# Kernel tuning notes

Hardware: AMD Instinct MI355X
Metric: run time of the kernel (lower is better)

Reference implementation:

```python
import jax, jax.numpy as jnp
import numpy as np

B, A, C, L, NH, SCALE = 1, 5, 64, 4, 8, 2
H = W = 24
S = 2 * C
KS = 5


def layernorm(x, g, b, eps=1e-5):
    m = x.mean(-1, keepdims=True)
    v = ((x - m) ** 2).mean(-1, keepdims=True)
    return (x - m) * jax.lax.rsqrt(v + eps) * g + b


def pe_1d(n, d):
    # PositionEncoding: temperature**(2*(i//2)/d), sin of even cols then cos of odd cols
    g = jnp.arange(d, dtype=jnp.float32)
    g = 10000.0 ** (2.0 * jnp.floor(g / 2.0) / d)
    p = jnp.arange(n, dtype=jnp.float32)[:, None] / g[None, :]
    return jnp.concatenate([jnp.sin(p[:, 0::2]), jnp.cos(p[:, 1::2])], axis=1)  # [n, d]


def mha(qk, v, in_w, out_w, nh, mask=None):
    # qk, v: [Lq, Bt, D]; torch nn.MultiheadAttention, bias-free, q=k=qk, value=v
    Lq, Bt, D = qk.shape
    dh = D // nh
    wq, wk, wv = jnp.split(in_w, 3, axis=0)
    q = (qk @ wq.T).reshape(Lq, Bt, nh, dh)
    k = (qk @ wk.T).reshape(Lq, Bt, nh, dh)
    vv = (v @ wv.T).reshape(Lq, Bt, nh, dh)
    s = jnp.einsum('lbhd,mbhd->bhlm', q, k) / jnp.sqrt(jnp.float32(dh))
    if mask is not None:
        s = s + mask
    a = jax.nn.softmax(s, axis=-1)
    o = jnp.einsum('bhlm,mbhd->lbhd', a, vv).reshape(Lq, Bt, D)
    return o @ out_w.T


def unfold3x3(x):
    # F.unfold(k=3, pad=1).permute(2,0,1): [N,c,h,w] -> [h*w, N, 9c] (c, kh, kw ordering)
    N, c, h, w = x.shape
    xp = jnp.pad(x, ((0, 0), (0, 0), (1, 1), (1, 1)))
    p = jnp.stack([xp[:, :, i:i + h, j:j + w] for i in range(3) for j in range(3)], axis=2)
    return p.reshape(N, c * 9, h * w).transpose(2, 0, 1)


def conv_hw(x5, w):
    # Conv3d kernel (1,3,3) pad (0,1,1): 2D conv per angular view
    Bc, Ci, Aa, h, w_ = x5.shape
    y = jax.lax.conv_general_dilated(
        x5.transpose(0, 2, 1, 3, 4).reshape(Bc * Aa, Ci, h, w_), w, (1, 1), ((1, 1), (1, 1)),
        dimension_numbers=('NCHW', 'OIHW', 'NCHW'))
    return y.reshape(Bc, Aa, w.shape[0], h, w_).transpose(0, 2, 1, 3, 4)


def window_mask(h, w, k):
    # SpaTrans.gen_mask: additive -inf outside a k x k local window
    kl, kr = k // 2, k - k // 2
    i = jnp.arange(h)
    j = jnp.arange(w)
    mh = (i[None, :] >= i[:, None] - kl) & (i[None, :] < i[:, None] + kr)
    mw = (j[None, :] >= j[:, None] - kl) & (j[None, :] < j[:, None] + kr)
    m = (mh[:, None, :, None] & mw[None, :, None, :]).reshape(h * w, h * w)
    return jnp.where(m, 0.0, -jnp.inf).astype(jnp.float32)


def setup_inputs() -> dict:
    key = jax.random.key(0)
    ks = iter(jax.random.split(key, 64))
    def nrm(shape, s=0.02):
        return jax.random.normal(next(ks), shape, dtype=jnp.float32) * s
    d = {}
    d['lr'] = jax.random.normal(next(ks), (B, 1, A * H, A * W), dtype=jnp.float32)
    Hh, Wh = H * SCALE, W * SCALE
    ch = -1.0 + (2.0 * jnp.arange(Hh, dtype=jnp.float32) + 1.0) / Hh
    cw = -1.0 + (2.0 * jnp.arange(Wh, dtype=jnp.float32) + 1.0) / Wh
    g = jnp.stack(jnp.meshgrid(ch, cw, indexing='ij'), axis=-1).reshape(-1, 2)
    d['coord'] = jnp.broadcast_to(g, (B, Hh * Wh, 2))
    d['conv0_w'] = nrm((C, 1, 3, 3), 0.1)
    d['convi_w'] = nrm((3, C, C, 3, 3), 0.05)
    d['ang_ln_g'] = jnp.ones((L, C)); d['ang_ln_b'] = jnp.zeros((L, C))
    d['ang_in'] = nrm((L, 3 * C, C)); d['ang_out'] = nrm((L, C, C))
    d['ang_ff_g'] = jnp.ones((L, C)); d['ang_ff_b'] = jnp.zeros((L, C))
    d['ang_w1'] = nrm((L, 2 * C, C)); d['ang_w2'] = nrm((L, C, 2 * C))
    d['spa_mlp'] = nrm((L, S, 9 * C))
    d['spa_ln_g'] = jnp.ones((L, S)); d['spa_ln_b'] = jnp.zeros((L, S))
    d['spa_in'] = nrm((L, 3 * S, S)); d['spa_out'] = nrm((L, S, S))
    d['spa_ff_g'] = jnp.ones((L, S)); d['spa_ff_b'] = jnp.zeros((L, S))
    d['spa_w1'] = nrm((L, 2 * S, S)); d['spa_w2'] = nrm((L, S, 2 * S))
    d['spa_lin'] = nrm((L, C, S))
    IN = A * A * C + 2 + 2 * A * A
    d['imp_w0'] = nrm((320, IN)); d['imp_b0'] = jnp.zeros((320,))
    d['imp_w1'] = nrm((320, 320)); d['imp_b1'] = jnp.zeros((320,))
    d['imp_w2'] = nrm((3 * A * A, 320)); d['imp_b2'] = jnp.zeros((3 * A * A,))
    return d


def reference(lr, coord, conv0_w, convi_w, ang_ln_g, ang_ln_b, ang_in, ang_out,
              ang_ff_g, ang_ff_b, ang_w1, ang_w2, spa_mlp, spa_ln_g, spa_ln_b,
              spa_in, spa_out, spa_ff_g, spa_ff_b, spa_w1, spa_w2, spa_lin,
              imp_w0, imp_b0, imp_w1, imp_b1, imp_w2, imp_b2):
    Bn = lr.shape[0]
    # 'b c (a1 h) (a2 w) -> b c (a1 a2) h w'
    x = lr.reshape(Bn, 1, A, H, A, W).transpose(0, 1, 2, 4, 3, 5).reshape(Bn, 1, A * A, H, W)
    spa_pe_img = ((pe_1d(H, C)[:, None, :] + pe_1d(W, C)[None, :, :]) * 0.5).transpose(2, 0, 1)[None]  # [1,C,h,w]
    ang_pe = pe_1d(A * A, C)[:, None, :]  # [A^2,1,C]
    buf = conv_hw(x, conv0_w)
    t = buf
    for i in range(3):
        t = jax.nn.leaky_relu(conv_hw(t, convi_w[i]), 0.2)
    buf = t + buf
    mask = window_mask(H, W, KS)
    blk = buf
    for l in range(L):
        # ---- AngTrans: tokens [A^2, B*h*w, C]
        tok = blk.transpose(2, 0, 3, 4, 1).reshape(A * A, Bn * H * W, C)
        tn = layernorm(tok + ang_pe, ang_ln_g[l], ang_ln_b[l])
        tok = mha(tn, tok, ang_in[l], ang_out[l], NH) + tok
        ff = layernorm(tok, ang_ff_g[l], ang_ff_b[l])
        tok = jax.nn.relu(ff @ ang_w1[l].T) @ ang_w2[l].T + tok
        blk = tok.reshape(A * A, Bn, H, W, C).transpose(1, 4, 0, 2, 3)
        # ---- SpaTrans: tokens [h*w, B*A^2, 2C] with local-window mask
        xb = blk.transpose(0, 2, 1, 3, 4).reshape(Bn * A * A, C, H, W)
        tok = unfold3x3(xb) @ spa_mlp[l].T
        pe_tok = unfold3x3(spa_pe_img) @ spa_mlp[l].T
        tn = layernorm(tok + pe_tok, spa_ln_g[l], spa_ln_b[l])
        tok = mha(tn, tok, spa_in[l], spa_out[l], NH, mask) + tok
        ff = layernorm(tok, spa_ff_g[l], spa_ff_b[l])
        tok = jax.nn.relu(ff @ spa_w1[l].T) @ spa_w2[l].T + tok
        t5 = tok.reshape(H, W, Bn, A * A, S).transpose(2, 4, 3, 0, 1)  # b s a h w
        blk = jnp.einsum('os,bsahw->boahw', spa_lin[l], t5)  # 1x1x1 Conv3d
    buf = blk + buf
    # 'b c (a1 a2) h w -> b c (a1 h) (a2 w)'
    feat_lr = buf.reshape(Bn, C, A, A, H, W).transpose(0, 1, 2, 4, 3, 5).reshape(Bn, C, A * H, A * W)
    Hh, Wh = H * SCALE, W * SCALE
    # per-view bilinear upsample (align_corners=False)
    v = feat_lr.reshape(Bn, C, A, H, A, W).transpose(0, 2, 4, 1, 3, 5).reshape(Bn * A * A, C, H, W)
    v = jax.image.resize(v, (Bn * A * A, C, Hh, Wh), method='bilinear')
    feat_hr = v.reshape(Bn, A, A, C, Hh, Wh).transpose(0, 4, 5, 1, 2, 3).reshape(Bn, Hh, Wh, A * A * C)
    # nearest grid_sample of LR cell-center coords -> relative coord
    c_ = jnp.clip(coord + 1e-6, -1 + 1e-6, 1 - 1e-6)
    ih = jnp.clip(jnp.round(((c_[..., 0] + 1) * H - 1) / 2), 0, H - 1)
    iw = jnp.clip(jnp.round(((c_[..., 1] + 1) * W - 1) / 2), 0, W - 1)
    qh = -1.0 + (2.0 * ih + 1.0) / H
    qw = -1.0 + (2.0 * iw + 1.0) / W
    rel = jnp.stack([(coord[..., 0] - qh) * H, (coord[..., 1] - qw) * W], axis=-1).reshape(Bn, Hh, Wh, 2)
    au = 0.5 + jnp.arange(A, dtype=jnp.float32)  # make_coord ranges [0,A]
    ca = jnp.stack(jnp.meshgrid(au, au, indexing='ij'), axis=-1).reshape(-1)
    ca = jnp.broadcast_to(ca, (Bn, Hh, Wh, 2 * A * A))
    inp = jnp.concatenate([feat_hr, rel, ca], axis=-1)
    h0 = jax.nn.relu(inp @ imp_w0.T + imp_b0)
    h1 = jax.nn.relu(h0 @ imp_w1.T + imp_b1)
    o = h1 @ imp_w2.T + imp_b2
    # 'b h w (a1 a2 c) -> b c (a1 h) (a2 w)', c=3
    return o.reshape(Bn, Hh, Wh, A, A, 3).transpose(0, 5, 3, 1, 4, 2).reshape(Bn, 3, A * Hh, A * Wh)
```

## Files before the change

kernel.cpp:

```cpp
#include <hip/hip_runtime.h>
#include <math.h>

typedef short  s16x4 __attribute__((ext_vector_type(4)));
typedef short  s16x8 __attribute__((ext_vector_type(8)));
typedef float  f32x4 __attribute__((ext_vector_type(4)));

static const size_t PE25_  = 0;
static const size_t SPAPE_ = 2048;
static const size_t X_     = 38912;
static const size_t CAV_   = 53312;
static const size_t PETOK_ = 54272;
static const size_t W9C_   = 349184;
static const size_t W9S_   = 459776;
static const size_t BUF_   = 754688;
static const size_t BLK_   = 1676288;
static const size_t ATOK_  = 2597888;
static const size_t TNF_   = 3519488;
static const size_t STOK_  = 4441088;
static const size_t STOK2_ = 6284288;
static const size_t QKV_   = 9970688;
static const size_t WS_FLOATS = 15500288;
static const size_t T0_ = QKV_ + 2764800;
static const size_t T1_ = T0_ + 921600;
static const size_t ZP_ = QKV_;
static const size_t H0_ = STOK_;
static const size_t H1_ = STOK2_;

__device__ inline ushort f2bf(float x) {
  unsigned u = __float_as_uint(x);
  u += 0x7fffu + ((u >> 16) & 1u);
  return (ushort)(u >> 16);
}
__device__ inline float bf2f(ushort h) { return __uint_as_float(((unsigned)h) << 16); }

__device__ inline void store_split(char* p, f32x4 v) {
  s16x4 hi, lo;
  #pragma unroll
  for (int e = 0; e < 4; ++e) {
    float x = v[e];
    ushort h = f2bf(x);
    ushort l = f2bf(x - bf2f(h));
    hi[e] = (short)h; lo[e] = (short)l;
  }
  *(s16x4*)p = hi;
  *(s16x4*)(p + 1024) = lo;
}

__device__ inline void scatter_split(char* base, int rr, int c6, float v) {
  ushort hi = f2bf(v);
  ushort lo = f2bf(v - bf2f(hi));
  int ks = c6 >> 5, kh = (c6 >> 4) & 1, k4 = (c6 >> 2) & 3;
  int lane2 = (k4 >> 1)*32 + ((rr & 15) << 1) + (k4 & 1);
  int byt = (((rr >> 4)*2 + ks) << 11) + (kh << 9) + (lane2 << 3) + (c6 & 3)*2;
  *(ushort*)(base + byt) = hi;
  *(ushort*)(base + byt + 1024) = lo;
}

__device__ inline void ld_bf16x16(const ushort* p, float* dst) {
  s16x8 a = *(const s16x8*)p;
  s16x8 b = *(const s16x8*)(p + 8);
  #pragma unroll
  for (int e = 0; e < 8; ++e) { dst[e] = bf2f((ushort)a[e]); dst[8 + e] = bf2f((ushort)b[e]); }
}

__device__ inline void slot_decode(int i, int wave, int lane,
                                   int& row, int& kof, int& wo) {
  int idx = (i << 2) + wave;
  int msub = idx >> 2, ks = (idx >> 1) & 1, kh = idx & 1;
  int rsub = (lane >> 1) & 15;
  int ksub = ((lane >> 5) << 3) + ((lane & 1) << 2);
  row = (msub << 4) + rsub;
  kof = (ks << 5) + (kh << 4) + ksub;
  wo = ((msub * 2 + ks) << 11) + (kh << 9) + (lane << 3);
}

__device__ inline void mfma_step(const char* ldsA, const char* ldsB, int lane,
                                 int wr, int wc, f32x4 acc[2][2]) {
  #pragma unroll
  for (int ks = 0; ks < 2; ++ks) {
    s16x8 ah[2], al[2], bh[2], bl[2];
    #pragma unroll
    for (int i = 0; i < 2; ++i) {
      const char* pa = ldsA + (((wr*2 + i)*2 + ks) << 11) + (lane << 4);
      ah[i] = *(const s16x8*)pa;
      al[i] = *(const s16x8*)(pa + 1024);
      const char* pb = ldsB + (((wc*2 + i)*2 + ks) << 11) + (lane << 4);
      bh[i] = *(const s16x8*)pb;
      bl[i] = *(const s16x8*)(pb + 1024);
    }
    #pragma unroll
    for (int i = 0; i < 2; ++i) {
      #pragma unroll
      for (int j = 0; j < 2; ++j) {
        acc[i][j] = __builtin_amdgcn_mfma_f32_16x16x32_bf16(ah[i], bh[j], acc[i][j], 0, 0, 0);
        acc[i][j] = __builtin_amdgcn_mfma_f32_16x16x32_bf16(ah[i], bl[j], acc[i][j], 0, 0, 0);
        acc[i][j] = __builtin_amdgcn_mfma_f32_16x16x32_bf16(al[i], bh[j], acc[i][j], 0, 0, 0);
      }
    }
  }
}

__device__ inline void epilogue(f32x4 acc[2][2], const float* bias, const float* res,
                                float* out, int N, int m0, int n0,
                                int wr, int wc, int lane, int act) {
  int colb = n0 + wc*32 + (lane & 15);
  int rowb = m0 + wr*32 + ((lane >> 4) << 2);
  #pragma unroll
  for (int j = 0; j < 2; ++j) {
    int cc = colb + j*16;
    if (cc >= N) continue;
    float bv = bias ? bias[cc] : 0.f;
    #pragma unroll
    for (int i = 0; i < 2; ++i) {
      #pragma unroll
      for (int r = 0; r < 4; ++r) {
        int rr = rowb + i*16 + r;
        float v = acc[i][j][r] + bv;
        if (act == 1) v = fmaxf(v, 0.f);
        else if (act == 2) v = v > 0.f ? v : 0.2f*v;
        if (res) v += res[(long)rr*N + cc];
        if (act == 3) {
          int hh = rr / 48, ww2 = rr % 48, q = cc / 3, ch = cc % 3;
          out[ch*57600 + ((q/5)*48 + hh)*240 + (q%5)*48 + ww2] = v;
        } else if (act == 4) {
          ((ushort*)out)[(long)rr*N + cc] = f2bf(v);
        } else {
          out[(long)rr*N + cc] = v;
        }
      }
    }
  }
}

template<int K>
__global__ __launch_bounds__(256) void qkvg_k(
    const float* __restrict__ A, const float* __restrict__ pe, int pe_mode,
    const float* __restrict__ g, const float* __restrict__ bb,
    const float* __restrict__ W, float* __restrict__ out,
    int NTr0, int NTr1, int N, int Mreal, int Mpad) {
  constexpr int NCH = K / 64;
  __shared__ char Apl[NCH * 16384];
  __shared__ char Bp[16384];
  __shared__ float sw_[4][64][2];
  __shared__ float sf_[64][2];
  int bid = blockIdx.x;
  int type = bid / Mpad, m = bid % Mpad;
  if (m >= Mreal) return;
  int m0 = m*64;
  int NTr = type ? NTr1 : NTr0;
  int ntbase = type ? NTr0 : 0;
  int t = threadIdx.x, lane = t & 63, wave = t >> 6;
  int wr = wave >> 1, wc = wave & 1;

  if (type == 0) {
    f32x4 rv[NCH][4];
    float sA[4], sQ[4];
    #pragma unroll
    for (int i = 0; i < 4; ++i) { sA[i] = 0.f; sQ[i] = 0.f; }
    #pragma unroll
    for (int ch = 0; ch < NCH; ++ch)
      #pragma unroll
      for (int i = 0; i < 4; ++i) {
        int row, kof, wo;
        slot_decode(i, wave, lane, row, kof, wo);
        int gk = ch*64 + kof;
        f32x4 av = *(const f32x4*)&A[(long)(m0 + row)*K + gk];
        if (pe_mode == 0)      av += *(const f32x4*)&pe[(long)(m0/576)*K + gk];
        else                   av += *(const f32x4*)&pe[(long)(m0%576 + row)*K + gk];
        rv[ch][i] = av;
        #pragma unroll
        for (int e = 0; e < 4; ++e) { sA[i] += av[e]; sQ[i] = fmaf(av[e], av[e], sQ[i]); }
      }
    #pragma unroll
    for (int i = 0; i < 4; ++i) {
      float s = sA[i], q = sQ[i];
      s += __shfl_xor(s, 1, 64);  q += __shfl_xor(q, 1, 64);
      s += __shfl_xor(s, 32, 64); q += __shfl_xor(q, 32, 64);
      if ((lane & 1) == 0 && lane < 32) {
        int row = i*16 + (lane >> 1);
        sw_[wave][row][0] = s; sw_[wave][row][1] = q;
      }
    }
    __syncthreads();
    if (t < 64) {
      float s = sw_[0][t][0] + sw_[1][t][0] + sw_[2][t][0] + sw_[3][t][0];
      float q = sw_[0][t][1] + sw_[1][t][1] + sw_[2][t][1] + sw_[3][t][1];
      float mean = s / K, var = q / K - mean*mean;
      sf_[t][0] = mean; sf_[t][1] = rsqrtf(var + 1e-5f);
    }
    __syncthreads();
    #pragma unroll
    for (int ch = 0; ch < NCH; ++ch)
      #pragma unroll
      for (int i = 0; i < 4; ++i) {
        int row, kof, wo;
        slot_decode(i, wave, lane, row, kof, wo);
        int gk = ch*64 + kof;
        float mean = sf_[row][0], rstd = sf_[row][1];
        f32x4 gv = *(const f32x4*)&g[gk];
        f32x4 bv = *(const f32x4*)&bb[gk];
        f32x4 nv;
        #pragma unroll
        for (int e = 0; e < 4; ++e) nv[e] = (rv[ch][i][e] - mean)*rstd*gv[e] + bv[e];
        store_split(Apl + ch*16384 + wo, nv);
      }
  } else {
    #pragma unroll
    for (int ch = 0; ch < NCH; ++ch)
      #pragma unroll
      for (int i = 0; i < 4; ++i) {
        int row, kof, wo;
        slot_decode(i, wave, lane, row, kof, wo);
        f32x4 av = *(const f32x4*)&A[(long)(m0 + row)*K + ch*64 + kof];
        store_split(Apl + ch*16384 + wo, av);
      }
  }

  int S = NTr * NCH;
  f32x4 pb[4];
  #pragma unroll
  for (int i = 0; i < 4; ++i) {
    int row, kof, wo;
    slot_decode(i, wave, lane, row, kof, wo);
    pb[i] = *(const f32x4*)&W[(long)(ntbase*64 + row)*K + kof];
  }
  f32x4 acc[2][2];
  #pragma unroll
  for (int i = 0; i < 2; ++i)
    #pragma unroll
    for (int j = 0; j < 2; ++j) acc[i][j] = (f32x4){0.f,0.f,0.f,0.f};
  for (int s = 0; s < S; ++s) {
    int nt = s / NCH, ch = s % NCH;
    __syncthreads();
    #pragma unroll
    for (int i = 0; i < 4; ++i) {
      int row, kof, wo;
      slot_decode(i, wave, lane, row, kof, wo);
      store_split(Bp + wo, pb[i]);
    }
    __syncthreads();
    if (s + 1 < S) {
      int ntn = (s+1) / NCH, chn = (s+1) % NCH;
      #pragma unroll
      for (int i = 0; i < 4; ++i) {
        int row, kof, wo;
        slot_decode(i, wave, lane, row, kof, wo);
        pb[i] = *(const f32x4*)&W[(long)((ntbase+ntn)*64 + row)*K + chn*64 + kof];
      }
    }
    mfma_step(Apl + ch*16384, Bp, lane, wr, wc, acc);
    if (ch == NCH - 1) {
      epilogue(acc, nullptr, nullptr, out, N, m0, (ntbase+nt)*64, wr, wc, lane, 4);
      #pragma unroll
      for (int i = 0; i < 2; ++i)
        #pragma unroll
        for (int j = 0; j < 2; ++j) acc[i][j] = (f32x4){0.f,0.f,0.f,0.f};
    }
  }
}

template<int K, int LN>
__global__ __launch_bounds__(256) void mgemm3_k(
    const float* __restrict__ A, const float* __restrict__ A2, int nsplit,
    const float* __restrict__ pe, int pe_mode,
    const float* __restrict__ g, const float* __restrict__ bb,
    const float* __restrict__ W, const float* __restrict__ bias,
    const float* __restrict__ res, float* __restrict__ out,
    int N, int act, int Mreal, int Mpad) {
  constexpr int NCH = K / 64;
  __shared__ char Apl[NCH * 16384];
  __shared__ char Bp[16384];
  int bid = blockIdx.x;
  int m = bid % Mpad, nt = bid / Mpad;
  if (m >= Mreal) return;
  int m0 = m*64, n0 = nt*64;
  int t = threadIdx.x, lane = t & 63, wave = t >> 6;
  int wr = wave >> 1, wc = wave & 1;
  const float* As = LN ? A2 : A;
  #pragma unroll
  for (int ch = 0; ch < NCH; ++ch)
    #pragma unroll
    for (int i = 0; i < 4; ++i) {
      int row, kof, wo;
      slot_decode(i, wave, lane, row, kof, wo);
      f32x4 av = *(const f32x4*)&As[(long)(m0 + row)*K + ch*64 + kof];
      store_split(Apl + ch*16384 + wo, av);
    }
  f32x4 pb[4];
  #pragma unroll
  for (int i = 0; i < 4; ++i) {
    int row, kof, wo;
    slot_decode(i, wave, lane, row, kof, wo);
    int br = n0 + row;
    pb[i] = (br < N) ? *(const f32x4*)&W[(long)br*K + kof] : (f32x4){0.f,0.f,0.f,0.f};
  }
  __syncthreads();
  f32x4 acc[2][2];
  #pragma unroll
  for (int i = 0; i < 2; ++i)
    #pragma unroll
    for (int j = 0; j < 2; ++j) acc[i][j] = (f32x4){0.f,0.f,0.f,0.f};
  for (int ch = 0; ch < NCH; ++ch) {
    #pragma unroll
    for (int i = 0; i < 4; ++i) {
      int row, kof, wo;
      slot_decode(i, wave, lane, row, kof, wo);
      store_split(Bp + wo, pb[i]);
    }
    __syncthreads();
    if (ch + 1 < NCH) {
      #pragma unroll
      for (int i = 0; i < 4; ++i) {
        int row, kof, wo;
        slot_decode(i, wave, lane, row, kof, wo);
        int br = n0 + row;
        pb[i] = (br < N) ? *(const f32x4*)&W[(long)br*K + (ch+1)*64 + kof]
                         : (f32x4){0.f,0.f,0.f,0.f};
      }
    }
    mfma_step(Apl + ch*16384, Bp, lane, wr, wc, acc);
    if (ch + 1 < NCH) __syncthreads();
  }
  epilogue(acc, bias, res, out, N, m0, n0, wr, wc, lane, act);
}

__global__ __launch_bounds__(256) void cgemm3_k(
    const float* __restrict__ in, const float* __restrict__ W9, long wstride,
    const float* __restrict__ res, float* __restrict__ out, long ostride,
    int N, int act, int Mreal, int Mpad) {
  __shared__ float halo[144 * 68];
  __shared__ char Ap[16384], Bp[16384];
  int bid = blockIdx.x;
  int m = bid % Mpad, nt = bid / Mpad;
  if (m >= Mreal) return;
  int ly = blockIdx.y;
  W9  += (long)ly * wstride;
  out += (long)ly * ostride;
  int m0 = m*64, n0 = nt*64;
  int a = m0 / 576, off = m0 % 576;
  int h_lo = off/24 - 1, h_hi = (off + 63)/24 + 1;
  int RH = h_hi - h_lo + 1;
  int t = threadIdx.x, lane = t & 63, wave = t >> 6;
  int wr = wave >> 1, wc = wave & 1;
  for (int sidx = t; sidx < RH*24*16; sidx += 256) {
    int tokr = sidx >> 4, c4 = (sidx & 15) << 2;
    int h = h_lo + tokr/24, w = tokr % 24;
    f32x4 v = {0.f,0.f,0.f,0.f};
    if ((unsigned)h < 24u) v = *(const f32x4*)&in[(long)(a*576 + h*24 + w)*64 + c4];
    *(f32x4*)&halo[tokr*68 + c4] = v;
  }
  f32x4 pb[4];
  #pragma unroll
  for (int i = 0; i < 4; ++i) {
    int row, kof, wo;
    slot_decode(i, wave, lane, row, kof, wo);
    int br = n0 + row;
    pb[i] = (br < N) ? *(const f32x4*)&W9[(long)br*64 + kof] : (f32x4){0.f,0.f,0.f,0.f};
  }
  __syncthreads();
  f32x4 acc[2][2];
  #pragma unroll
  for (int i = 0; i < 2; ++i)
    #pragma unroll
    for (int j = 0; j < 2; ++j) acc[i][j] = (f32x4){0.f,0.f,0.f,0.f};
  for (int ij = 0; ij < 9; ++ij) {
    int di = ij/3 - 1, dj = ij%3 - 1;
    #pragma unroll
    for (int i = 0; i < 4; ++i) {
      int row, kof, wo;
      slot_decode(i, wave, lane, row, kof, wo);
      int tok = off + row;
      int h2 = tok/24 + di, w2 = tok%24 + dj;
      f32x4 v = {0.f,0.f,0.f,0.f};
      if ((unsigned)h2 < 24u && (unsigned)w2 < 24u)
        v = *(const f32x4*)&halo[((h2 - h_lo)*24 + w2)*68 + kof];
      store_split(Ap + wo, v);
      store_split(Bp + wo, pb[i]);
    }
    __syncthreads();
    if (ij < 8) {
      #pragma unroll
      for (int i = 0; i < 4; ++i) {
        int row, kof, wo;
        slot_decode(i, wave, lane, row, kof, wo);
        int br = n0 + row;
        pb[i] = (br < N) ? *(const f32x4*)&W9[((long)(ij+1)*N + br)*64 + kof]
                         : (f32x4){0.f,0.f,0.f,0.f};
      }
    }
    mfma_step(Ap, Bp, lane, wr, wc, acc);
    if (ij < 8) __syncthreads();
  }
  epilogue(acc, nullptr, res, out, N, m0, n0, wr, wc, lane, act);
}

__global__ __launch_bounds__(256) void ang_mega_k(
    const ushort* __restrict__ qkv, const float* __restrict__ Wout,
    const float* __restrict__ blkr, const float* __restrict__ g,
    const float* __restrict__ bb, float* __restrict__ atok, float* __restrict__ tnf) {
  int hw = blockIdx.x;
  __shared__ float lq[25*192];
  __shared__ float lao[25*64];
  __shared__ float po[25*68];
  __shared__ float wout[64*65];
  __shared__ float st[25][2];
  int t = threadIdx.x;
  for (int idx = t; idx < 600; idx += 256) {
    int a3 = idx / 24, c8 = (idx % 24) * 8;
    s16x8 r = *(const s16x8*)&qkv[(long)(a3*576 + hw)*192 + c8];
    #pragma unroll
    for (int e = 0; e < 8; ++e) lq[a3*192 + c8 + e] = bf2f((ushort)r[e]);
  }
  for (int idx = t; idx < 4096; idx += 256) {
    int c = idx >> 6, d = idx & 63;
    wout[c*65 + d] = Wout[idx];
  }
  __syncthreads();
  if (t < 200) {
    int l = t / 8, head = t & 7;
    const float* q = lq + l*192 + head*8;
    float s[25]; float mx = -1e30f;
    #pragma unroll
    for (int mm = 0; mm < 25; ++mm) {
      const float* kk = lq + mm*192 + 64 + head*8;
      float acc = 0.f;
      #pragma unroll
      for (int d = 0; d < 8; ++d) acc = fmaf(q[d], kk[d], acc);
      acc *= 0.3535533905932738f;
      s[mm] = acc; mx = fmaxf(mx, acc);
    }
    float sum = 0.f;
    #pragma unroll
    for (int mm = 0; mm < 25; ++mm) { s[mm] = expf(s[mm] - mx); sum += s[mm]; }
    float inv = 1.f / sum;
    #pragma unroll
    for (int d = 0; d < 8; ++d) {
      float acc = 0.f;
      #pragma unroll
      for (int mm = 0; mm < 25; ++mm) acc = fmaf(s[mm], lq[mm*192 + 128 + head*8 + d], acc);
      lao[l*64 + head*8 + d] = acc * inv;
    }
  }
  __syncthreads();
  for (int idx = t; idx < 1600; idx += 256) {
    int tok = idx >> 6, c = idx & 63;
    const float* ar = &lao[tok*64];
    const float* wr = &wout[c*65];
    float accp = 0.f;
    #pragma unroll 16
    for (int d = 0; d < 64; ++d) accp = fmaf(ar[d], wr[d], accp);
    po[tok*68 + c] = accp + blkr[(long)(tok*576 + hw)*64 + c];
  }
  __syncthreads();
  if (t < 25) {
    float s = 0.f, q = 0.f;
    for (int c = 0; c < 64; ++c) { float x = po[t*68 + c]; s += x; q = fmaf(x, x, q); }
    float mean = s / 64.f, var = q / 64.f - mean*mean;
    st[t][0] = mean; st[t][1] = rsqrtf(var + 1e-5f);
  }
  __syncthreads();
  for (int idx = t; idx < 1600; idx += 256) {
    int tok = idx >> 6, c = idx & 63;
    float x = po[tok*68 + c];
    long gidx = (long)(tok*576 + hw)*64 + c;
    atok[gidx] = x;
    tnf[gidx] = (x - st[tok][0]) * st[tok][1] * g[c] + bb[c];
  }
}

__global__ __launch_bounds__(256) void ffn_ang_k(
    const float* __restrict__ tnf, const float* __restrict__ w1,
    const float* __restrict__ w2, float* __restrict__ atok,
    int Mreal, int Mpad) {
  __shared__ char Ap[16384], Bp[16384], Hp[2][16384];
  int bid = blockIdx.x;
  int m = bid % Mpad;
  if (m >= Mreal) return;
  int m0 = m*64;
  int t = threadIdx.x, lane = t & 63, wave = t >> 6;
  int wr = wave >> 1, wc = wave & 1;
  #pragma unroll
  for (int i = 0; i < 4; ++i) {
    int row, kof, wo;
    slot_decode(i, wave, lane, row, kof, wo);
    f32x4 av = *(const f32x4*)&tnf[(long)(m0 + row)*64 + kof];
    store_split(Ap + wo, av);
  }
  f32x4 pb[4];
  #pragma unroll
  for (int i = 0; i < 4; ++i) {
    int row, kof, wo;
    slot_decode(i, wave, lane, row, kof, wo);
    pb[i] = *(const f32x4*)&w1[(long)row*64 + kof];
  }
  __syncthreads();
  for (int nt = 0; nt < 2; ++nt) {
    #pragma unroll
    for (int i = 0; i < 4; ++i) {
      int row, kof, wo;
      slot_decode(i, wave, lane, row, kof, wo);
      store_split(Bp + wo, pb[i]);
    }
    __syncthreads();
    #pragma unroll
    for (int i = 0; i < 4; ++i) {
      int row, kof, wo;
      slot_decode(i, wave, lane, row, kof, wo);
      pb[i] = (nt == 0) ? *(const f32x4*)&w1[(long)(64 + row)*64 + kof]
                        : *(const f32x4*)&w2[(long)row*128 + kof];
    }
    f32x4 acc[2][2];
    #pragma unroll
    for (int i = 0; i < 2; ++i)
      #pragma unroll
      for (int j = 0; j < 2; ++j) acc[i][j] = (f32x4){0.f,0.f,0.f,0.f};
    mfma_step(Ap, Bp, lane, wr, wc, acc);
    #pragma unroll
    for (int jj = 0; jj < 2; ++jj)
      #pragma unroll
      for (int ii = 0; ii < 2; ++ii)
        #pragma unroll
        for (int r = 0; r < 4; ++r) {
          int rr = wr*32 + ii*16 + ((lane >> 4) << 2) + r;
          int cc = wc*32 + jj*16 + (lane & 15);
          scatter_split(Hp[nt], rr, cc, fmaxf(acc[ii][jj][r], 0.f));
        }
    __syncthreads();
  }
  f32x4 acc2[2][2];
  #pragma unroll
  for (int i = 0; i < 2; ++i)
    #pragma unroll
    for (int j = 0; j < 2; ++j) acc2[i][j] = (f32x4){0.f,0.f,0.f,0.f};
  for (int ch = 0; ch < 2; ++ch) {
    #pragma unroll
    for (int i = 0; i < 4; ++i) {
      int row, kof, wo;
      slot_decode(i, wave, lane, row, kof, wo);
      store_split(Bp + wo, pb[i]);
    }
    __syncthreads();
    if (ch == 0) {
      #pragma unroll
      for (int i = 0; i < 4; ++i) {
        int row, kof, wo;
        slot_decode(i, wave, lane, row, kof, wo);
        pb[i] = *(const f32x4*)&w2[(long)row*128 + 64 + kof];
      }
    }
    mfma_step(Hp[ch], Bp, lane, wr, wc, acc2);
    if (ch == 0) __syncthreads();
  }
  epilogue(acc2, nullptr, atok, atok, 64, m0, 0, wr, wc, lane, 0);
}

__global__ __launch_bounds__(512) void megaspa_k(
    const ushort* __restrict__ qkv, const float* __restrict__ stok,
    const float* __restrict__ wout, const float* __restrict__ g,
    const float* __restrict__ bb, const float* __restrict__ w1,
    const float* __restrict__ w2, const float* __restrict__ wlin,
    float* __restrict__ outb, int Mreal, int Mpad) {
  __shared__ char Aop[32768];
  __shared__ char SCR[65536];
  __shared__ float Rf[64*132];
  __shared__ float st[64][2];
  int bid = blockIdx.x;
  int m = bid % Mpad;
  if (m >= Mreal) return;
  int m0 = m*64;
  int t = threadIdx.x, lane = t & 63, wave = t >> 6;
  int wgrp = wave >> 2, w4 = wave & 3;
  int wr = w4 >> 1, wc = w4 & 1;
  char* Bp  = SCR + wgrp*16384;
  char* Hp0 = SCR + 32768;
  char* Hp1 = SCR + 49152;
  ushort* KV = (ushort*)SCR;

  for (int idx = t; idx < 2048; idx += 512) {
    int row = idx >> 5, c4 = (idx & 31) << 2;
    *(f32x4*)&Rf[row*132 + c4] = *(const f32x4*)&stok[(long)(m0 + row)*128 + c4];
  }

  int va = m0 / 576, off = m0 % 576;
  int hb = off/24 - 2;
  int he = (off + 63)/24 + 2;
  int RH = he - hb + 1;
  int rr1 = t >> 3, head = t & 7;
  int x = m0 + rr1;
  int hw = x % 576, h = hw / 24, w = hw % 24;
  float qr[16];
  ld_bf16x16(qkv + (long)x*384 + head*16, qr);
  for (int idx = t; idx < RH*24*16; idx += 512) {
    int tokr = idx >> 4, c8 = (idx & 15) << 3;
    int hh2 = hb + tokr/24, ww2 = tokr % 24;
    s16x8 vv = (s16x8){0,0,0,0,0,0,0,0};
    if ((unsigned)hh2 < 24u)
      vv = *(const s16x8*)&qkv[(long)(va*576 + hh2*24 + ww2)*384 + 128 + c8];
    *(s16x8*)&KV[tokr*136 + c8] = vv;
  }
  __syncthreads();
  float s[25]; float mx = -1e30f;
  #pragma unroll
  for (int ro = 0; ro < 5; ++ro) {
    int h2 = h + ro - 2;
    int hrow = h2 - hb;
    #pragma unroll
    for (int co = 0; co < 5; ++co) {
      int w2 = w + co - 2;
      int w2c = min(max(w2, 0), 23);
      const ushort* kp = &KV[(hrow*24 + w2c)*136 + head*16];
      s16x8 k0 = *(const s16x8*)kp;
      s16x8 k1 = *(const s16x8*)(kp + 8);
      float sc = -1e30f;
      if (h2 >= 0 && h2 < 24 && w2 >= 0 && w2 < 24) {
        sc = 0.f;
        #pragma unroll
        for (int d = 0; d < 8; ++d) sc = fmaf(qr[d], bf2f((ushort)k0[d]), sc);
        #pragma unroll
        for (int d = 0; d < 8; ++d) sc = fmaf(qr[8+d], bf2f((ushort)k1[d]), sc);
        sc *= 0.25f;
      }
      s[ro*5 + co] = sc; mx = fmaxf(mx, sc);
    }
  }
  float sum = 0.f;
  #pragma unroll
  for (int i = 0; i < 25; ++i) {
    float e = (s[i] > -1e29f) ? expf(s[i] - mx) : 0.f;
    s[i] = e; sum += e;
  }
  float inv = 1.f / sum;
  __syncthreads();
  for (int idx = t; idx < RH*24*16; idx += 512) {
    int tokr = idx >> 4, c8 = (idx & 15) << 3;
    int hh2 = hb + tokr/24, ww2 = tokr % 24;
    s16x8 vv = (s16x8){0,0,0,0,0,0,0,0};
    if ((unsigned)hh2 < 24u)
      vv = *(const s16x8*)&qkv[(long)(va*576 + hh2*24 + ww2)*384 + 256 + c8];
    *(s16x8*)&KV[tokr*136 + c8] = vv;
  }
  __syncthreads();
  {
    float acc[16];
    #pragma unroll
    for (int d = 0; d < 16; ++d) acc[d] = 0.f;
    #pragma unroll
    for (int ro = 0; ro < 5; ++ro) {
      int h2 = h + ro - 2;
      int hrow = h2 - hb;
      (void)h2;
      #pragma unroll
      for (int co = 0; co < 5; ++co) {
        int w2 = w + co - 2;
        int w2c = min(max(w2, 0), 23);
        const ushort* vp = &KV[(hrow*24 + w2c)*136 + head*16];
        s16x8 v0 = *(const s16x8*)vp;
        s16x8 v1 = *(const s16x8*)(vp + 8);
        float sv = s[ro*5 + co];
        #pragma unroll
        for (int d = 0; d < 8; ++d) acc[d] = fmaf(sv, bf2f((ushort)v0[d]), acc[d]);
        #pragma unroll
        for (int d = 0; d < 8; ++d) acc[8+d] = fmaf(sv, bf2f((ushort)v1[d]), acc[8+d]);
      }
    }
    #pragma unroll
    for (int d = 0; d < 16; ++d) {
      int cc = head*16 + d;
      scatter_split(Aop + (cc >> 6)*16384, rr1, cc & 63, acc[d] * inv);
    }
  }

  {
    int nt = wgrp;
    f32x4 acc[2][2];
    #pragma unroll
    for (int i = 0; i < 2; ++i)
      #pragma unroll
      for (int j = 0; j < 2; ++j) acc[i][j] = (f32x4){0.f,0.f,0.f,0.f};
    for (int ch = 0; ch < 2; ++ch) {
      __syncthreads();
      #pragma unroll
      for (int i = 0; i < 4; ++i) {
        int row, kof, wo;
        slot_decode(i, w4, lane, row, kof, wo);
        f32x4 bv = *(const f32x4*)&wout[(long)(nt*64 + row)*128 + ch*64 + kof];
        store_split(Bp + wo, bv);
      }
      __syncthreads();
      mfma_step(Aop + ch*16384, Bp, lane, wr, wc, acc);
    }
    int colb = nt*64 + wc*32 + (lane & 15);
    int rowb = wr*32 + ((lane >> 4) << 2);
    #pragma unroll
    for (int j = 0; j < 2; ++j)
      #pragma unroll
      for (int i = 0; i < 2; ++i)
        #pragma unroll
        for (int r = 0; r < 4; ++r) {
          int rr = rowb + i*16 + r, cc = colb + j*16;
          Rf[rr*132 + cc] += acc[i][j][r];
        }
  }
  __syncthreads();

  {
    int row = t >> 3, q8 = t & 7;
    const float* yr = &Rf[row*132 + q8*16];
    float sm = 0.f, sq = 0.f;
    #pragma unroll
    for (int j2 = 0; j2 < 16; ++j2) { float xv = yr[j2]; sm += xv; sq = fmaf(xv, xv, sq); }
    sm += __shfl_xor(sm, 1, 64); sq += __shfl_xor(sq, 1, 64);
    sm += __shfl_xor(sm, 2, 64); sq += __shfl_xor(sq, 2, 64);
    sm += __shfl_xor(sm, 4, 64); sq += __shfl_xor(sq, 4, 64);
    if (q8 == 0) {
      float mean = sm / 128.f, var = sq / 128.f - mean*mean;
      st[row][0] = mean; st[row][1] = rsqrtf(var + 1e-5f);
    }
  }
  __syncthreads();
  {
    int ch = wgrp;
    #pragma unroll
    for (int i = 0; i < 4; ++i) {
      int row, kof, wo;
      slot_decode(i, w4, lane, row, kof, wo);
      int gk = ch*64 + kof;
      f32x4 xv = *(const f32x4*)&Rf[row*132 + gk];
      float mean = st[row][0], rstd = st[row][1];
      f32x4 gv = *(const f32x4*)&g[gk];
      f32x4 bv = *(const f32x4*)&bb[gk];
      f32x4 nv;
      #pragma unroll
      for (int e = 0; e < 4; ++e) nv[e] = (xv[e] - mean)*rstd*gv[e] + bv[e];
      store_split(Aop + ch*16384 + wo, nv);
    }
  }

  f32x4 acc2[2][2];
  #pragma unroll
  for (int i = 0; i < 2; ++i)
    #pragma unroll
    for (int j = 0; j < 2; ++j) acc2[i][j] = (f32x4){0.f,0.f,0.f,0.f};
  for (int r = 0; r < 2; ++r) {
    int nt = 2*r + wgrp;
    f32x4 accH[2][2];
    #pragma unroll
    for (int i = 0; i < 2; ++i)
      #pragma unroll
      for (int j = 0; j < 2; ++j) accH[i][j] = (f32x4){0.f,0.f,0.f,0.f};
    for (int ch = 0; ch < 2; ++ch) {
      __syncthreads();
      #pragma unroll
      for (int i = 0; i < 4; ++i) {
        int row, kof, wo;
        slot_decode(i, w4, lane, row, kof, wo);
        f32x4 bv = *(const f32x4*)&w1[(long)(nt*64 + row)*128 + ch*64 + kof];
        store_split(Bp + wo, bv);
      }
      __syncthreads();
      mfma_step(Aop + ch*16384, Bp, lane, wr, wc, accH);
    }
    char* Hpw = wgrp ? Hp1 : Hp0;
    #pragma unroll
    for (int jj = 0; jj < 2; ++jj)
      #pragma unroll
      for (int ii = 0; ii < 2; ++ii)
        #pragma unroll
        for (int rx = 0; rx < 4; ++rx) {
          int rr = wr*32 + ii*16 + ((lane >> 4) << 2) + rx;
          int cc = wc*32 + jj*16 + (lane & 15);
          scatter_split(Hpw, rr, cc, fmaxf(accH[ii][jj][rx], 0.f));
        }
    for (int q = 0; q < 2; ++q) {
      __syncthreads();
      #pragma unroll
      for (int i = 0; i < 4; ++i) {
        int row, kof, wo;
        slot_decode(i, w4, lane, row, kof, wo);
        f32x4 bv = *(const f32x4*)&w2[(long)(wgrp*64 + row)*256 + (2*r + q)*64 + kof];
        store_split(Bp + wo, bv);
      }
      __syncthreads();
      mfma_step(q ? Hp1 : Hp0, Bp, lane, wr, wc, acc2);
    }
  }
  {
    int colb = wc*32 + (lane & 15);
    int rowb = wr*32 + ((lane >> 4) << 2);
    #pragma unroll
    for (int jj = 0; jj < 2; ++jj)
      #pragma unroll
      for (int ii = 0; ii < 2; ++ii)
        #pragma unroll
        for (int rx = 0; rx < 4; ++rx) {
          int rr = rowb + ii*16 + rx;
          int cc = colb + jj*16;
          scatter_split(Aop + wgrp*16384, rr, cc,
                        acc2[ii][jj][rx] + Rf[rr*132 + wgrp*64 + cc]);
        }
  }

  f32x4 acc3[2][2];
  #pragma unroll
  for (int i = 0; i < 2; ++i)
    #pragma unroll
    for (int j = 0; j < 2; ++j) acc3[i][j] = (f32x4){0.f,0.f,0.f,0.f};
  for (int ch = 0; ch < 2; ++ch) {
    __syncthreads();
    if (wgrp == 0) {
      #pragma unroll
      for (int i = 0; i < 4; ++i) {
        int row, kof, wo;
        slot_decode(i, w4, lane, row, kof, wo);
        f32x4 bv = *(const f32x4*)&wlin[(long)row*128 + ch*64 + kof];
        store_split(SCR + wo, bv);
      }
    }
    __syncthreads();
    if (wgrp == 0) mfma_step(Aop + ch*16384, SCR, lane, wr, wc, acc3);
  }
  if (wgrp == 0)
    epilogue(acc3, nullptr, nullptr, outb, 64, m0, 0, wr, wc, lane, 0);
}

__global__ __launch_bounds__(256) void zgemm3_k(
    const float* __restrict__ buf, const float* __restrict__ blk,
    const float* __restrict__ W0, float* __restrict__ Zp) {
  __shared__ char Ap[16384], Bp[16384];
  int bid = blockIdx.x;
  int m = bid % 9;
  int nz = bid / 9;
  int n = nz % 5, z = nz / 5;
  int m0 = m*64, n0 = n*64;
  int t = threadIdx.x, lane = t & 63, wave = t >> 6;
  int wr = wave >> 1, wc = wave & 1;
  f32x4 pa[4], pb[4];
  #pragma unroll
  for (int i = 0; i < 4; ++i) {
    int row, kof, wo;
    slot_decode(i, wave, lane, row, kof, wo);
    long tok = (long)(z*5)*576 + m0 + row;
    pa[i] = *(const f32x4*)&buf[tok*64 + kof];
    pa[i] += *(const f32x4*)&blk[tok*64 + kof];
    pb[i] = *(const f32x4*)&W0[(long)(n0 + row)*1652 + (z*5)*64 + kof];
  }
  f32x4 acc[2][2];
  #pragma unroll
  for (int i = 0; i < 2; ++i)
    #pragma unroll
    for (int j = 0; j < 2; ++j) acc[i][j] = (f32x4){0.f,0.f,0.f,0.f};
  for (int q = 0; q < 5; ++q) {
    #pragma unroll
    for (int i = 0; i < 4; ++i) {
      int row, kof, wo;
      slot_decode(i, wave, lane, row, kof, wo);
      store_split(Ap + wo, pa[i]);
      store_split(Bp + wo, pb[i]);
    }
    __syncthreads();
    if (q < 4) {
      #pragma unroll
      for (int i = 0; i < 4; ++i) {
        int row, kof, wo;
        slot_decode(i, wave, lane, row, kof, wo);
        long tok = (long)(z*5 + q + 1)*576 + m0 + row;
        pa[i] = *(const f32x4*)&buf[tok*64 + kof];
        pa[i] += *(const f32x4*)&blk[tok*64 + kof];
        pb[i] = *(const f32x4*)&W0[(long)(n0 + row)*1652 + (z*5 + q + 1)*64 + kof];
      }
    }
    mfma_step(Ap, Bp, lane, wr, wc, acc);
    if (q < 4) __syncthreads();
  }
  epilogue(acc, nullptr, nullptr, Zp + (long)z*184320, 320, m0, n0, wr, wc, lane, 0);
}

__global__ void combine_k(const float* __restrict__ Zp, const float* __restrict__ cav,
                          const float* __restrict__ coord, float* __restrict__ h0out) {
  int gidx = blockIdx.x * 256 + threadIdx.x;
  if (gidx >= 2304 * 320) return;
  int p = gidx / 320, o = gidx % 320;
  int hh = p / 48, ww = p % 48;
  float sh = hh * 0.5f - 0.25f, sw = ww * 0.5f - 0.25f;
  int h0i = (int)floorf(sh); float fh = sh - h0i;
  int w0i = (int)floorf(sw); float fw = sw - w0i;
  int h0c = max(h0i, 0), h1c = min(h0i + 1, 23);
  int w0c = max(w0i, 0), w1c = min(w0i + 1, 23);
  int i00 = (h0c*24 + w0c)*320 + o, i01 = (h0c*24 + w1c)*320 + o;
  int i10 = (h1c*24 + w0c)*320 + o, i11 = (h1c*24 + w1c)*320 + o;
  float z00 = 0.f, z01 = 0.f, z10 = 0.f, z11 = 0.f;
  #pragma unroll
  for (int z = 0; z < 5; ++z) {
    const float* Zz = Zp + (long)z*184320;
    z00 += Zz[i00]; z01 += Zz[i01]; z10 += Zz[i10]; z11 += Zz[i11];
  }
  float v = (1.f-fh)*((1.f-fw)*z00 + fw*z01) + fh*((1.f-fw)*z10 + fw*z11);
  #pragma unroll
  for (int d = 0; d < 2; ++d) {
    float co = coord[p*2 + d];
    float cc = fminf(fmaxf(co + 1e-6f, -1.f + 1e-6f), 1.f - 1e-6f);
    float ix = rintf(((cc + 1.f)*24.f - 1.f)*0.5f);
    ix = fminf(fmaxf(ix, 0.f), 23.f);
    float q = -1.f + (2.f*ix + 1.f)/24.f;
    v = fmaf((co - q)*24.f, cav[320*(d+1) + o], v);
  }
  h0out[gidx] = fmaxf(v + cav[o], 0.f);
}

__device__ inline float pe_val(int pos, int c) {
  int j = c & 31;
  float freq = powf(10000.f, -2.f * (float)j / 64.f);
  float arg = (float)pos * freq;
  return (c < 32) ? sinf(arg) : cosf(arg);
}

__global__ void setup_k(const float* __restrict__ lr, const float* __restrict__ convi_w,
                        const float* __restrict__ spa_mlp,
                        const float* __restrict__ imp_w0, const float* __restrict__ imp_b0,
                        float* pe25, float* spa_pe, float* X, float* w9c, float* w9s,
                        float* cav) {
  int g = blockIdx.x * 256 + threadIdx.x;
  if (g < 1600) { pe25[g] = pe_val(g >> 6, g & 63); return; }
  g -= 1600;
  if (g < 36864) {
    int hw = g >> 6, c = g & 63; int h = hw / 24, w = hw % 24;
    spa_pe[g] = 0.5f * (pe_val(h, c) + pe_val(w, c)); return;
  }
  g -= 36864;
  if (g < 14400) {
    int aa = g / 576, hw = g % 576, h = hw / 24, w = hw % 24;
    X[g] = lr[((aa/5)*24 + h)*120 + (aa%5)*24 + w]; return;
  }
  g -= 14400;
  if (g < 110592) {
    int cv = g / 36864, rem = g % 36864;
    int ij = rem / 4096, oc = rem % 4096;
    int o = oc >> 6, c = oc & 63;
    w9c[g] = convi_w[((long)(cv*64 + o)*64 + c)*9 + ij]; return;
  }
  g -= 110592;
  if (g < 294912) {
    int l = g / 73728, rem = g % 73728;
    int ij = rem / 8192, oc = rem % 8192;
    int o = oc >> 6, c = oc & 63;
    w9s[g] = spa_mlp[((long)(l*128 + o))*576 + c*9 + ij]; return;
  }
  g -= 294912;
  if (g < 320) {
    int o = g;
    float s = imp_b0[o];
    #pragma unroll
    for (int idx = 0; idx < 50; ++idx) {
      int pair = idx >> 1;
      float cvv = 0.5f + (float)((idx & 1) ? pair % 5 : pair / 5);
      s = fmaf(cvv, imp_w0[(long)o*1652 + 1602 + idx], s);
    }
    cav[o] = s;
    cav[320 + o] = imp_w0[(long)o*1652 + 1600];
    cav[640 + o] = imp_w0[(long)o*1652 + 1601];
  }
}

__global__ void conv0_k(const float* __restrict__ X, const float* __restrict__ W,
                        float* __restrict__ out) {
  int sp = threadIdx.x >> 6, lane = threadIdx.x & 63;
  int strip = blockIdx.x * 4 + sp;
  int a = strip / 48, r = strip % 48, h = r >> 1, w0 = (r & 1) * 12;
  __shared__ float patch[4][3][16];
  if (lane < 42) {
    int i = lane / 14, col = lane % 14;
    int h2 = h + i - 1, w2 = w0 + col - 1;
    float v = 0.f;
    if ((unsigned)h2 < 24u && (unsigned)w2 < 24u) v = X[a*576 + h2*24 + w2];
    patch[sp][i][col] = v;
  }
  __syncthreads();
  float wv[9];
  #pragma unroll
  for (int q = 0; q < 9; ++q) wv[q] = W[lane*9 + q];
  #pragma unroll
  for (int p = 0; p < 12; ++p) {
    float acc = 0.f;
    #pragma unroll
    for (int i = 0; i < 3; ++i)
      #pragma unroll
      for (int j = 0; j < 3; ++j)
        acc = fmaf(patch[sp][i][p + j], wv[i*3 + j], acc);
    out[(long)(a*576 + h*24 + w0 + p)*64 + lane] = acc;
  }
}

extern "C" void kernel_launch(void* const* d_in, const int* in_sizes, int n_in,
                              void* d_out, int out_size, void* d_ws, size_t ws_size,
                              hipStream_t stream) {
  (void)in_sizes; (void)n_in; (void)out_size;
  if (ws_size < (size_t)WS_FLOATS * 4) return;
  float* ws = (float*)d_ws;

  const float* lr       = (const float*)d_in[0];
  const float* coord    = (const float*)d_in[1];
  const float* conv0_w  = (const float*)d_in[2];
  const float* convi_w  = (const float*)d_in[3];
  const float* ang_ln_g = (const float*)d_in[4];
  const float* ang_ln_b = (const float*)d_in[5];
  const float* ang_in   = (const float*)d_in[6];
  const float* ang_out  = (const float*)d_in[7];
  const float* ang_ff_g = (const float*)d_in[8];
  const float* ang_ff_b = (const float*)d_in[9];
  const float* ang_w1   = (const float*)d_in[10];
  const float* ang_w2   = (const float*)d_in[11];
  const float* spa_mlp  = (const float*)d_in[12];
  const float* spa_ln_g = (const float*)d_in[13];
  const float* spa_ln_b = (const float*)d_in[14];
  const float* spa_in   = (const float*)d_in[15];
  const float* spa_out  = (const float*)d_in[16];
  const float* spa_ff_g = (const float*)d_in[17];
  const float* spa_ff_b = (const float*)d_in[18];
  const float* spa_w1   = (const float*)d_in[19];
  const float* spa_w2   = (const float*)d_in[20];
  const float* spa_lin  = (const float*)d_in[21];
  const float* imp_w0   = (const float*)d_in[22];
  const float* imp_b0   = (const float*)d_in[23];
  const float* imp_w1   = (const float*)d_in[24];
  const float* imp_b1   = (const float*)d_in[25];
  const float* imp_w2   = (const float*)d_in[26];
  const float* imp_b2   = (const float*)d_in[27];

  float* pe25 = ws + PE25_;  float* spa_pe = ws + SPAPE_;  float* X = ws + X_;
  float* cav = ws + CAV_;    float* petok = ws + PETOK_;
  float* w9c = ws + W9C_;    float* w9s = ws + W9S_;
  float* buf = ws + BUF_;    float* blk = ws + BLK_;      float* atok = ws + ATOK_;
  float* tnf = ws + TNF_;    float* stok = ws + STOK_;
  float* qkvf = ws + QKV_;   ushort* qkvh = (ushort*)(ws + QKV_);
  float* t0 = ws + T0_;      float* t1 = ws + T1_;
  float* Zp = ws + ZP_;      float* h0 = ws + H0_;        float* h1 = ws + H1_;

  setup_k<<<1792, 256, 0, stream>>>(lr, convi_w, spa_mlp, imp_w0, imp_b0,
                                    pe25, spa_pe, X, w9c, w9s, cav);
  conv0_k<<<300, 256, 0, stream>>>(X, conv0_w, buf);
  cgemm3_k<<<dim3(232,1), 256, 0, stream>>>(buf, w9c,         0, nullptr, t0,  0, 64, 2, 225, 232);
  cgemm3_k<<<dim3(232,1), 256, 0, stream>>>(t0,  w9c + 36864, 0, nullptr, t1,  0, 64, 2, 225, 232);
  cgemm3_k<<<dim3(232,1), 256, 0, stream>>>(t1,  w9c + 73728, 0, buf,     buf, 0, 64, 2, 225, 232);
  cgemm3_k<<<dim3(32, 4), 256, 0, stream>>>(spa_pe, w9s, 73728, nullptr, petok, 73728,
                                            128, 0, 9, 16);

  for (int l = 0; l < 4; ++l) {
    const float* blkr = (l == 0) ? buf : blk;
    qkvg_k<64><<<464, 256, 0, stream>>>(blkr, pe25, 0,
        ang_ln_g + l*64, ang_ln_b + l*64, ang_in + l*192*64, qkvf,
        2, 1, 192, 225, 232);
    ang_mega_k<<<576, 256, 0, stream>>>(qkvh, ang_out + l*64*64, blkr,
        ang_ff_g + l*64, ang_ff_b + l*64, atok, tnf);
    ffn_ang_k<<<232, 256, 0, stream>>>(tnf, ang_w1 + l*128*64, ang_w2 + l*64*128,
        atok, 225, 232);
    cgemm3_k<<<dim3(464,1), 256, 0, stream>>>(atok, w9s + l*73728, 0, nullptr, stok, 0,
        128, 0, 225, 232);
    qkvg_k<128><<<464, 256, 0, stream>>>(stok, petok + l*73728, 1,
        spa_ln_g + l*128, spa_ln_b + l*128, spa_in + l*384*128, qkvf,
        4, 2, 384, 225, 232);
    megaspa_k<<<232, 512, 0, stream>>>(qkvh, stok, spa_out + l*128*128,
        spa_ff_g + l*128, spa_ff_b + l*128, spa_w1 + l*256*128, spa_w2 + l*128*256,
        spa_lin + l*64*128, blk, 225, 232);
  }

  zgemm3_k<<<225, 256, 0, stream>>>(buf, blk, imp_w0, Zp);
  combine_k<<<2880, 256, 0, stream>>>(Zp, cav, coord, h0);
  mgemm3_k<320,0><<<200, 256, 0, stream>>>(h0, h0, 0, nullptr, -1, nullptr, nullptr,
      imp_w1, imp_b1, nullptr, h1, 320, 1, 36, 40);
  mgemm3_k<320,0><<<80, 256, 0, stream>>>(h1, h1, 0, nullptr, -1, nullptr, nullptr,
      imp_w2, imp_b2, nullptr, (float*)d_out, 75, 3, 36, 40);
}
```

Baseline: 558.2 us.

## Read window K/V directly from global memory and prefetch out-proj weights

The local-window attention no longer stages K and V rows into shared memory. Each thread now loads its 5x5 neighbourhood K/V vectors straight from global memory, relying on cache reuse, which removes two staging loops and their barriers. The out-projection weight tiles are also preloaded into registers before the attention so their global latency overlaps with compute. The cost is redundant global/L2 traffic, since neighbouring threads fetch the same K/V rows, plus higher register pressure from holding the prefetched weights and the per-row K/V arrays.

```diff
diff --git a/kernel.cpp b/kernel.cpp
--- a/kernel.cpp
+++ b/kernel.cpp
@@ -574,93 +574,83 @@
   char* Bp  = SCR + wgrp*16384;
   char* Hp0 = SCR + 32768;
   char* Hp1 = SCR + 49152;
-  ushort* KV = (ushort*)SCR;
 
   for (int idx = t; idx < 2048; idx += 512) {
     int row = idx >> 5, c4 = (idx & 31) << 2;
     *(f32x4*)&Rf[row*132 + c4] = *(const f32x4*)&stok[(long)(m0 + row)*128 + c4];
   }
-
-  int va = m0 / 576, off = m0 % 576;
-  int hb = off/24 - 2;
-  int he = (off + 63)/24 + 2;
-  int RH = he - hb + 1;
-  int rr1 = t >> 3, head = t & 7;
-  int x = m0 + rr1;
-  int hw = x % 576, h = hw / 24, w = hw % 24;
-  float qr[16];
-  ld_bf16x16(qkv + (long)x*384 + head*16, qr);
-  for (int idx = t; idx < RH*24*16; idx += 512) {
-    int tokr = idx >> 4, c8 = (idx & 15) << 3;
-    int hh2 = hb + tokr/24, ww2 = tokr % 24;
-    s16x8 vv = (s16x8){0,0,0,0,0,0,0,0};
-    if ((unsigned)hh2 < 24u)
-      vv = *(const s16x8*)&qkv[(long)(va*576 + hh2*24 + ww2)*384 + 128 + c8];
-    *(s16x8*)&KV[tokr*136 + c8] = vv;
-  }
-  __syncthreads();
-  float s[25]; float mx = -1e30f;
-  #pragma unroll
-  for (int ro = 0; ro < 5; ++ro) {
-    int h2 = h + ro - 2;
-    int hrow = h2 - hb;
-    #pragma unroll
-    for (int co = 0; co < 5; ++co) {
-      int w2 = w + co - 2;
-      int w2c = min(max(w2, 0), 23);
-      const ushort* kp = &KV[(hrow*24 + w2c)*136 + head*16];
-      s16x8 k0 = *(const s16x8*)kp;
-      s16x8 k1 = *(const s16x8*)(kp + 8);
-      float sc = -1e30f;
-      if (h2 >= 0 && h2 < 24 && w2 >= 0 && w2 < 24) {
-        sc = 0.f;
-        #pragma unroll
-        for (int d = 0; d < 8; ++d) sc = fmaf(qr[d], bf2f((ushort)k0[d]), sc);
-        #pragma unroll
-        for (int d = 0; d < 8; ++d) sc = fmaf(qr[8+d], bf2f((ushort)k1[d]), sc);
-        sc *= 0.25f;
-      }
-      s[ro*5 + co] = sc; mx = fmaxf(mx, sc);
-    }
-  }
-  float sum = 0.f;
-  #pragma unroll
-  for (int i = 0; i < 25; ++i) {
-    float e = (s[i] > -1e29f) ? expf(s[i] - mx) : 0.f;
-    s[i] = e; sum += e;
-  }
-  float inv = 1.f / sum;
-  __syncthreads();
-  for (int idx = t; idx < RH*24*16; idx += 512) {
-    int tokr = idx >> 4, c8 = (idx & 15) << 3;
-    int hh2 = hb + tokr/24, ww2 = tokr % 24;
-    s16x8 vv = (s16x8){0,0,0,0,0,0,0,0};
-    if ((unsigned)hh2 < 24u)
-      vv = *(const s16x8*)&qkv[(long)(va*576 + hh2*24 + ww2)*384 + 256 + c8];
-    *(s16x8*)&KV[tokr*136 + c8] = vv;
-  }
-  __syncthreads();
+  f32x4 pw[2][4];
+  #pragma unroll
+  for (int ch = 0; ch < 2; ++ch)
+    #pragma unroll
+    for (int i = 0; i < 4; ++i) {
+      int row, kof, wo;
+      slot_decode(i, w4, lane, row, kof, wo);
+      pw[ch][i] = *(const f32x4*)&wout[(long)(wgrp*64 + row)*128 + ch*64 + kof];
+    }
+
   {
-    float acc[16];
-    #pragma unroll
-    for (int d = 0; d < 16; ++d) acc[d] = 0.f;
+    int rr1 = t >> 3, head = t & 7;
+    int x = m0 + rr1;
+    int hw = x % 576, h = hw / 24, w = hw % 24;
+    float qr[16];
+    ld_bf16x16(qkv + (long)x*384 + head*16, qr);
+    float s[25]; float mx = -1e30f;
     #pragma unroll
     for (int ro = 0; ro < 5; ++ro) {
       int h2 = h + ro - 2;
-      int hrow = h2 - hb;
-      (void)h2;
+      s16x8 k0[5], k1[5];
       #pragma unroll
       for (int co = 0; co < 5; ++co) {
-        int w2 = w + co - 2;
-        int w2c = min(max(w2, 0), 23);
-        const ushort* vp = &KV[(hrow*24 + w2c)*136 + head*16];
-        s16x8 v0 = *(const s16x8*)vp;
-        s16x8 v1 = *(const s16x8*)(vp + 8);
+        int xt = x + (ro - 2)*24 + (co - 2);
+        xt = min(max(xt, 0), 14399);
+        const ushort* kp = qkv + (long)xt*384 + 128 + head*16;
+        k0[co] = *(const s16x8*)kp;
+        k1[co] = *(const s16x8*)(kp + 8);
+      }
+      #pragma unroll
+      for (int co = 0; co < 5; ++co) {
+        int w2c = w + co - 2;
+        float sc = -1e30f;
+        if (h2 >= 0 && h2 < 24 && w2c >= 0 && w2c < 24) {
+          sc = 0.f;
+          #pragma unroll
+          for (int d = 0; d < 8; ++d) sc = fmaf(qr[d], bf2f((ushort)k0[co][d]), sc);
+          #pragma unroll
+          for (int d = 0; d < 8; ++d) sc = fmaf(qr[8+d], bf2f((ushort)k1[co][d]), sc);
+          sc *= 0.25f;
+        }
+        s[ro*5 + co] = sc; mx = fmaxf(mx, sc);
+      }
+    }
+    float sum = 0.f;
+    #pragma unroll
+    for (int i = 0; i < 25; ++i) {
+      float e = (s[i] > -1e29f) ? expf(s[i] - mx) : 0.f;
+      s[i] = e; sum += e;
+    }
+    float inv = 1.f / sum;
+    float acc[16];
+    #pragma unroll
+    for (int d = 0; d < 16; ++d) acc[d] = 0.f;
+    #pragma unroll
+    for (int ro = 0; ro < 5; ++ro) {
+      s16x8 v0[5], v1[5];
+      #pragma unroll
+      for (int co = 0; co < 5; ++co) {
+        int xt = x + (ro - 2)*24 + (co - 2);
+        xt = min(max(xt, 0), 14399);
+        const ushort* vp = qkv + (long)xt*384 + 256 + head*16;
+        v0[co] = *(const s16x8*)vp;
+        v1[co] = *(const s16x8*)(vp + 8);
+      }
+      #pragma unroll
+      for (int co = 0; co < 5; ++co) {
         float sv = s[ro*5 + co];
         #pragma unroll
-        for (int d = 0; d < 8; ++d) acc[d] = fmaf(sv, bf2f((ushort)v0[d]), acc[d]);
+        for (int d = 0; d < 8; ++d) acc[d] = fmaf(sv, bf2f((ushort)v0[co][d]), acc[d]);
         #pragma unroll
-        for (int d = 0; d < 8; ++d) acc[8+d] = fmaf(sv, bf2f((ushort)v1[d]), acc[8+d]);
+        for (int d = 0; d < 8; ++d) acc[8+d] = fmaf(sv, bf2f((ushort)v1[co][d]), acc[8+d]);
       }
     }
     #pragma unroll
@@ -683,8 +673,7 @@
       for (int i = 0; i < 4; ++i) {
         int row, kof, wo;
         slot_decode(i, w4, lane, row, kof, wo);
-        f32x4 bv = *(const f32x4*)&wout[(long)(nt*64 + row)*128 + ch*64 + kof];
-        store_split(Bp + wo, bv);
+        store_split(Bp + wo, pw[ch][i]);
       }
       __syncthreads();
       mfma_step(Aop + ch*16384, Bp, lane, wr, wc, acc);
```

Result: no change. 553.8 us, median of 2 (-0.8%).
